# Optimization experiments

Measured on AMD Instinct MI355X. Metric: run time of the kernel, lower is better.

Reference implementation:

```python
import jax, jax.numpy as jnp
import numpy as np

N_NODES = 5000
N_EDGES = 50000
BATCH = 8
SEQ = 12
IN_CH = 2
HID = 64
OUT_CH = 1
K = 3
N_LAYERS = 2


def setup_inputs() -> dict:
    key = jax.random.key(0)
    ks = jax.random.split(key, 20)
    d = {}
    d["x"] = jax.random.normal(ks[0], (BATCH, SEQ, N_NODES, IN_CH), dtype=jnp.float32)
    d["edge_index"] = jax.random.randint(ks[1], (2, N_EDGES), 0, N_NODES, dtype=jnp.int32)

    def w(k, fin):
        return jax.random.normal(k, (2, K, fin, HID), dtype=jnp.float32) * 0.05

    fins = [IN_CH + HID, HID + HID]
    i = 2
    for l in range(N_LAYERS):
        for g in ("z", "r", "h"):
            d["W" + g + str(l)] = w(ks[i], fins[l]); i += 1
            d["b" + g + str(l)] = jnp.zeros((HID,), jnp.float32)
    d["Wo"] = jax.random.normal(ks[i], (HID, OUT_CH), dtype=jnp.float32) * 0.05
    d["bo"] = jnp.zeros((OUT_CH,), jnp.float32)
    return d


def reference(x, edge_index,
              Wz0, bz0, Wr0, br0, Wh0, bh0,
              Wz1, bz1, Wr1, br1, Wh1, bh1,
              Wo, bo):
    B, T, N, _ = x.shape
    src, dst = edge_index[0], edge_index[1]
    ones = jnp.ones(src.shape, x.dtype)
    deg_out = jax.ops.segment_sum(ones, src, num_segments=N)
    deg_in = jax.ops.segment_sum(ones, dst, num_segments=N)
    inv = lambda dgr: jnp.where(dgr > 0, 1.0 / dgr, 0.0)
    norm_out = inv(deg_out)[src]  # [E], 1/deg_out(src)
    norm_in = inv(deg_in)[dst]    # [E], 1/deg_in(dst)

    def prop(X, norm):
        # X: [N, B, F] -> sparse matvec via gather/scatter
        msg = norm[:, None, None] * X[src]
        return jax.ops.segment_sum(msg, dst, num_segments=N)

    def dconv(X, W, b):
        # X: [N, B, Fin]; W: [2, K, Fin, H]; dual-direction Chebyshev diffusion
        H = jnp.einsum('nbf,fh->nbh', X, W[0, 0] + W[1, 0])
        Tx0o = Tx0i = X
        Tx1o = prop(X, norm_out)
        Tx1i = prop(X, norm_in)
        H = H + jnp.einsum('nbf,fh->nbh', Tx1o, W[0, 1]) \
              + jnp.einsum('nbf,fh->nbh', Tx1i, W[1, 1])
        for k in range(2, W.shape[1]):
            Tx2o = 2.0 * prop(Tx1o, norm_out) - Tx0o
            Tx2i = 2.0 * prop(Tx1i, norm_in) - Tx0i
            H = H + jnp.einsum('nbf,fh->nbh', Tx2o, W[0, k]) \
                  + jnp.einsum('nbf,fh->nbh', Tx2i, W[1, k])
            Tx0o, Tx1o = Tx1o, Tx2o
            Tx0i, Tx1i = Tx1i, Tx2i
        return H + b

    def cell(Xin, H, p):
        Wz, bz, Wr, br, Wh, bh = p
        XH = jnp.concatenate([Xin, H], axis=-1)
        Z = jax.nn.sigmoid(dconv(XH, Wz, bz))
        R = jax.nn.sigmoid(dconv(XH, Wr, br))
        Ht = jnp.tanh(dconv(jnp.concatenate([Xin, H * R], axis=-1), Wh, bh))
        return Z * H + (1.0 - Z) * Ht

    layers = [(Wz0, bz0, Wr0, br0, Wh0, bh0), (Wz1, bz1, Wr1, br1, Wh1, bh1)]
    hid = Wo.shape[0]
    h0 = jnp.zeros((len(layers), N, B, hid), x.dtype)
    xs = jnp.transpose(x, (1, 2, 0, 3))  # [T, N, B, F]

    def step(h, xt):
        inp = xt
        new_h = []
        for l, p in enumerate(layers):
            hl = cell(inp, h[l], p)
            new_h.append(hl)
            inp = hl
        h = jnp.stack(new_h)
        out = jnp.einsum('nbh,ho->nbo', h[-1], Wo) + bo
        return h, out

    _, outs = jax.lax.scan(step, h0, xs)      # [T, N, B, O]
    return jnp.transpose(outs, (2, 0, 1, 3))  # [B, T, N, O]
```

## Files before the change

### kernel.cpp

```cpp
#include <hip/hip_runtime.h>
#include <math.h>

#define NNODES 5000
#define NEDGES 50000
#define SEQT 12
#define NB 40000
#define MAXDEG 128

typedef __attribute__((ext_vector_type(8))) _Float16 half8;
typedef __attribute__((ext_vector_type(2))) _Float16 half2v;
typedef __attribute__((ext_vector_type(4))) float f32x4;


__global__ void count_deg_k(const int* __restrict__ ei, int* deg_out, int* deg_in){
    int e = blockIdx.x*blockDim.x + threadIdx.x;
    if (e < NEDGES){
        atomicAdd(&deg_out[ei[e]], 1);
        atomicAdd(&deg_in[ei[NEDGES + e]], 1);
    }
}

__global__ void scan_k(const int* __restrict__ deg_in, int* __restrict__ row_ptr){
    __shared__ int part[256];
    int tid = threadIdx.x;
// ... 69 lines not shown
    int kb = ks*32 + ((lane>>4)<<3);
    size_t o = ((size_t)(ks*4 + cf)*64 + lane)*8;
    for (int j=0;j<8;j++){
        int k = kb + j;
        float v = 0.f;
        if (ks == 0){
            if (k < 10) v = wfetch(W, 66, k>>1, k&1, col);
        } else {
            int slot = (ks-1)>>1;
            int f = 2 + k - 32 - 64*slot;
            v = wfetch(W, 66, slot, f, col);
        }
        wh[o+j] = (_Float16)v;
    }
}

__global__ void pack_l1_k(const float* __restrict__ W, _Float16* __restrict__ wh){
    int idx = blockIdx.x*256 + threadIdx.x;
    if (idx >= 4*20*64) return;
    int lane = idx & 63, rest = idx >> 6;
    int ks = rest % 20, cf = rest / 20;
    int col = cf*16 + (lane & 15);
    int kb = ks*32 + ((lane>>4)<<3);
    int slot = ks >> 2;
    size_t o = ((size_t)(ks*4 + cf)*64 + lane)*8;
    for (int j=0;j<8;j++){
        int k = kb + j;
        int f = k - slot*128;
        wh[o+j] = (_Float16)wfetch(W, 128, slot, f, col);
    }
}


template<int WH>
__global__ __launch_bounds__(WH) void k_dualh(
    const _Float16* __restrict__ S,
    _Float16* __restrict__ Yo, _Float16* __restrict__ Yi,
    const int* __restrict__ rp, const int* __restrict__ cs,
    const float* __restrict__ cwo, const float* __restrict__ cwi){
    constexpr int SLAB = 8*WH;
    int n = blockIdx.x;
    int beg = rp[n], deg = rp[n+1]-beg;
    int nst = deg < MAXDEG ? deg : MAXDEG;
    __shared__ int s_o[MAXDEG]; __shared__ float swo[MAXDEG], swi[MAXDEG];
    for (int j=threadIdx.x; j<nst; j+=WH){
        s_o[j] = cs[beg+j]*SLAB;
        swo[j] = cwo[beg+j]; swi[j] = cwi[beg+j];
    }
    __syncthreads();
    int off = threadIdx.x*8;
    float ao[8] = {0,0,0,0,0,0,0,0}, ai[8] = {0,0,0,0,0,0,0,0};
    for (int j=0;j<nst;j++){
        half8 v = *(const half8*)(S + s_o[j] + off);
        float wo=swo[j], wi=swi[j];
        #pragma unroll
        for (int e=0;e<8;e++){
            float xv = (float)v[e];
            ao[e]=fmaf(wo,xv,ao[e]); ai[e]=fmaf(wi,xv,ai[e]);
        }
    }
    for (int j=nst;j<deg;j++){
        half8 v = *(const half8*)(S + (size_t)cs[beg+j]*SLAB + off);
        float wo=cwo[beg+j], wi=cwi[beg+j];
        #pragma unroll
        for (int e=0;e<8;e++){
            float xv = (float)v[e];
            ao[e]=fmaf(wo,xv,ao[e]); ai[e]=fmaf(wi,xv,ai[e]);
        }
    }
    half8 po, pi;
    #pragma unroll
    for (int e=0;e<8;e++){ po[e]=(_Float16)ao[e]; pi[e]=(_Float16)ai[e]; }
    *(half8*)(Yo + (size_t)n*SLAB + off) = po;
    *(half8*)(Yi + (size_t)n*SLAB + off) = pi;
}

template<int WH>
__global__ __launch_bounds__(WH) void k_prop2h(
    const _Float16* __restrict__ T1o, const _Float16* __restrict__ T1i,
    _Float16* __restrict__ U2o, _Float16* __restrict__ U2i,
    const int* __restrict__ rp, const int* __restrict__ cs,
    const float* __restrict__ cwo, const float* __restrict__ cwi){
    constexpr int SLAB = 8*WH;
    int bx = blockIdx.x;
    int n = bx >> 1, sel = bx & 1;
    const _Float16* S = sel ? T1i : T1o;
    _Float16* U = sel ? U2i : U2o;
    const float* cw = sel ? cwi : cwo;
    int beg = rp[n], deg = rp[n+1]-beg;
    int nst = deg < MAXDEG ? deg : MAXDEG;
    __shared__ int s_o[MAXDEG]; __shared__ float s_w[MAXDEG];
    for (int j=threadIdx.x; j<nst; j+=WH){
        s_o[j] = cs[beg+j]*SLAB;
        s_w[j] = cw[beg+j];
    }
    __syncthreads();
    int off = threadIdx.x*8;
    float a[8] = {0,0,0,0,0,0,0,0};
    for (int j=0;j<nst;j++){
        half8 v = *(const half8*)(S + s_o[j] + off);
        float w=s_w[j];
        #pragma unroll
        for (int e=0;e<8;e++) a[e]=fmaf(w,(float)v[e],a[e]);
    }
    for (int j=nst;j<deg;j++){
        half8 v = *(const half8*)(S + (size_t)cs[beg+j]*SLAB + off);
        float w=cw[beg+j];
        #pragma unroll
        for (int e=0;e<8;e++) a[e]=fmaf(w,(float)v[e],a[e]);
    }
    half8 p;
    #pragma unroll
    for (int e=0;e<8;e++) p[e]=(_Float16)a[e];
    *(half8*)(U + (size_t)n*SLAB + off) = p;
}

__global__ __launch_bounds__(64) void k_dual_l0zrh(
    const _Float16* __restrict__ h0h, const _Float16* __restrict__ Xt,
    _Float16* __restrict__ T1o, _Float16* __restrict__ T1i, _Float16* __restrict__ XTh,
    const int* __restrict__ rp, const int* __restrict__ cs,
    const float* __restrict__ cwo, const float* __restrict__ cwi){
    int n = blockIdx.x;
    int beg = rp[n], deg = rp[n+1]-beg;
    int nst = deg < MAXDEG ? deg : MAXDEG;
    __shared__ int s_o[MAXDEG]; __shared__ float swo[MAXDEG], swi[MAXDEG];
    for (int j=threadIdx.x; j<nst; j+=64){
        s_o[j] = cs[beg+j]*512;
        swo[j] = cwo[beg+j]; swi[j] = cwi[beg+j];
    }
    __syncthreads();
    int off = threadIdx.x*8;
    {
        float ao[8] = {0,0,0,0,0,0,0,0}, ai[8] = {0,0,0,0,0,0,0,0};
        for (int j=0;j<nst;j++){
            half8 v = *(const half8*)(h0h + s_o[j] + off);
            float wo=swo[j], wi=swi[j];
            #pragma unroll
            for (int e=0;e<8;e++){
                float xv = (float)v[e];
                ao[e]=fmaf(wo,xv,ao[e]); ai[e]=fmaf(wi,xv,ai[e]);
            }
        }
        for (int j=nst;j<deg;j++){
            half8 v = *(const half8*)(h0h + (size_t)cs[beg+j]*512 + off);
            float wo=cwo[beg+j], wi=cwi[beg+j];
            #pragma unroll
            for (int e=0;e<8;e++){
                float xv = (float)v[e];
                ao[e]=fmaf(wo,xv,ao[e]); ai[e]=fmaf(wi,xv,ai[e]);
            }
        }
        half8 po, pi;
        #pragma unroll
        for (int e=0;e<8;e++){ po[e]=(_Float16)ao[e]; pi[e]=(_Float16)ai[e]; }
        *(half8*)(T1o + (size_t)n*512 + off) = po;
        *(half8*)(T1i + (size_t)n*512 + off) = pi;
    }
    if (threadIdx.x < 8){
        int b = threadIdx.x;
        float ax0=0,ax1=0, ay0=0,ay1=0;
        for (int j=0;j<nst;j++){
            int src = s_o[j] >> 9;
            half2v v = *(const half2v*)(Xt + src*16 + b*2);
            float x0=(float)v[0], x1=(float)v[1];
            ax0=fmaf(swo[j],x0,ax0); ax1=fmaf(swo[j],x1,ax1);
            ay0=fmaf(swi[j],x0,ay0); ay1=fmaf(swi[j],x1,ay1);
        }
        for (int j=nst;j<deg;j++){
            int src = cs[beg+j];
            half2v v = *(const half2v*)(Xt + src*16 + b*2);
            float x0=(float)v[0], x1=(float)v[1];
            ax0=fmaf(cwo[beg+j],x0,ax0); ax1=fmaf(cwo[beg+j],x1,ax1);
            ay0=fmaf(cwi[beg+j],x0,ay0); ay1=fmaf(cwi[beg+j],x1,ay1);
        }
        size_t ro = (size_t)(n*8 + b)*32;
        XTh[ro+0] = Xt[(size_t)(n*8+b)*2+0];
        XTh[ro+1] = Xt[(size_t)(n*8+b)*2+1];
        XTh[ro+2] = (_Float16)ax0; XTh[ro+3] = (_Float16)ax1;
        XTh[ro+4] = (_Float16)ay0; XTh[ro+5] = (_Float16)ay1;
    }
}

__global__ __launch_bounds__(64) void k_prop2_l0zrh(
    const _Float16* __restrict__ T1o, const _Float16* __restrict__ T1i,
    _Float16* __restrict__ T2o, _Float16* __restrict__ T2i, _Float16* __restrict__ XTh,
    const int* __restrict__ rp, const int* __restrict__ cs,
    const float* __restrict__ cwo, const float* __restrict__ cwi){
    int bx = blockIdx.x;
    int n = bx >> 1, sel = bx & 1;
    const _Float16* S = sel ? T1i : T1o;
    _Float16* U = sel ? T2i : T2o;
    const float* cw = sel ? cwi : cwo;
    int beg = rp[n], deg = rp[n+1]-beg;
    int nst = deg < MAXDEG ? deg : MAXDEG;
    __shared__ int s_o[MAXDEG]; __shared__ float s_w[MAXDEG];
    for (int j=threadIdx.x; j<nst; j+=64){
        s_o[j] = cs[beg+j]*512;
        s_w[j] = cw[beg+j];
    }
    __syncthreads();
    int off = threadIdx.x*8;
    {
        float a[8] = {0,0,0,0,0,0,0,0};
        for (int j=0;j<nst;j++){
            half8 v = *(const half8*)(S + s_o[j] + off);
            float w=s_w[j];
            #pragma unroll
            for (int e=0;e<8;e++) a[e]=fmaf(w,(float)v[e],a[e]);
        }
        for (int j=nst;j<deg;j++){
            half8 v = *(const half8*)(S + (size_t)cs[beg+j]*512 + off);
            float w=cw[beg+j];
            #pragma unroll
            for (int e=0;e<8;e++) a[e]=fmaf(w,(float)v[e],a[e]);
        }
        half8 p;
        #pragma unroll
        for (int e=0;e<8;e++) p[e]=(_Float16)a[e];
        *(half8*)(U + (size_t)n*512 + off) = p;
    }
    if (threadIdx.x < 8){
        int b = threadIdx.x;
        int xo = 2 + 2*sel;
        float a0=0,a1=0;
        for (int j=0;j<nst;j++){
            int src = s_o[j] >> 9;
            half2v v = *(const half2v*)(XTh + (size_t)src*256 + b*32 + xo);
            a0=fmaf(s_w[j],(float)v[0],a0); a1=fmaf(s_w[j],(float)v[1],a1);
        }
        for (int j=nst;j<deg;j++){
            int src = cs[beg+j];
            half2v v = *(const half2v*)(XTh + (size_t)src*256 + b*32 + xo);
            a0=fmaf(cw[beg+j],(float)v[0],a0); a1=fmaf(cw[beg+j],(float)v[1],a1);
        }
        size_t ro = (size_t)(n*8 + b)*32 + 6 + 2*sel;
        XTh[ro+0] = (_Float16)a0; XTh[ro+1] = (_Float16)a1;
    }
}

__global__ __launch_bounds__(128) void k_dual2x64h(
    const _Float16* __restrict__ h0h, const _Float16* __restrict__ h1h,
    _Float16* __restrict__ T1o, _Float16* __restrict__ T1i,
    const int* __restrict__ rp, const int* __restrict__ cs,
    const float* __restrict__ cwo, const float* __restrict__ cwi){
    int n = blockIdx.x;
    int beg = rp[n], deg = rp[n+1]-beg;
    int nst = deg < MAXDEG ? deg : MAXDEG;
    __shared__ int s_o[MAXDEG]; __shared__ float swo[MAXDEG], swi[MAXDEG];
    for (int j=threadIdx.x; j<nst; j+=128){
        s_o[j] = cs[beg+j]*512;
        swo[j] = cwo[beg+j]; swi[j] = cwi[beg+j];
    }
    __syncthreads();
    int off = threadIdx.x*8;
    int b = off >> 7, c = off & 127;
    const _Float16* S = (c < 64) ? h0h : h1h;
    int soff = b*64 + (c & 63);
    float ao[8] = {0,0,0,0,0,0,0,0}, ai[8] = {0,0,0,0,0,0,0,0};
    for (int j=0;j<nst;j++){
        half8 v = *(const half8*)(S + s_o[j] + soff);
        float wo=swo[j], wi=swi[j];
        #pragma unroll
        for (int e=0;e<8;e++){
            float xv = (float)v[e];
            ao[e]=fmaf(wo,xv,ao[e]); ai[e]=fmaf(wi,xv,ai[e]);
        }
    }
    for (int j=nst;j<deg;j++){
        half8 v = *(const half8*)(S + (size_t)cs[beg+j]*512 + soff);
        float wo=cwo[beg+j], wi=cwi[beg+j];
        #pragma unroll
        for (int e=0;e<8;e++){
            float xv = (float)v[e];
            ao[e]=fmaf(wo,xv,ao[e]); ai[e]=fmaf(wi,xv,ai[e]);
        }
    }
    half8 po, pi;
    #pragma unroll
    for (int e=0;e<8;e++){ po[e]=(_Float16)ao[e]; pi[e]=(_Float16)ai[e]; }
    *(half8*)(T1o + (size_t)n*1024 + off) = po;
    *(half8*)(T1i + (size_t)n*1024 + off) = pi;
}


struct KD { const _Float16* a; int st; };
struct GA { KD kd[20]; };

template<int NK, int NG, int EPI>
__global__ __launch_bounds__(256) void k_gemm(GA ga,
    const _Float16* __restrict__ wh0, const float* __restrict__ b0,
    const _Float16* __restrict__ wh1, const float* __restrict__ b1,
    float* __restrict__ Z, _Float16* __restrict__ Gout,
    float* __restrict__ Hf, _Float16* __restrict__ Hh,
    const float* __restrict__ Wo, const float* __restrict__ bo,
    float* __restrict__ out, int t){
    __shared__ _Float16 ldsb[2][NG*2048];
    __shared__ float spr[4][32];
    const int tid = threadIdx.x;
    const int lane = tid & 63, wv = tid >> 6, rl = lane & 15, kg = lane >> 4;
    const int m0 = blockIdx.x*64 + (wv&1)*32;
    const int cfb = (wv>>1)*2;
    const _Float16* wsrc[2] = {wh0, wh1};

    half8 srg[NG];
    half8 a0, a1, a0n, a1n;

    auto sload = [&](int ks){
        #pragma unroll
        for (int j=0;j<NG;j++)
            srg[j] = *(const half8*)(wsrc[j] + (size_t)ks*2048 + tid*8);
    };
    auto swrite = [&](int buf){
        #pragma unroll
        for (int j=0;j<NG;j++)
            *(half8*)&ldsb[buf][j*2048 + tid*8] = srg[j];
    };
    auto aload = [&](int ks, half8& x0, half8& x1){
        const _Float16* base = ga.kd[ks].a;
        const int st = ga.kd[ks].st;
        x0 = *(const half8*)(base + (size_t)(m0+rl)*st + kg*8);
        x1 = *(const half8*)(base + (size_t)(m0+16+rl)*st + kg*8);
    };

    f32x4 acc[NG][2][2];
    #pragma unroll
    for (int g=0; g<NG; ++g)
        #pragma unroll
        for (int cc=0; cc<2; ++cc)
            #pragma unroll
            for (int mr=0; mr<2; ++mr){
                acc[g][cc][mr][0]=0.f; acc[g][cc][mr][1]=0.f;
                acc[g][cc][mr][2]=0.f; acc[g][cc][mr][3]=0.f;
            }

    sload(0); swrite(0);
    if (NK>1) sload(1);
    aload(0, a0, a1);
    __syncthreads();
    for (int ks=0; ks<NK; ++ks){
        const int cur = ks & 1;
        if (ks+1 < NK){ swrite(cur^1); aload(ks+1, a0n, a1n); }
        if (ks+2 < NK) sload(ks+2);
        #pragma unroll
        for (int g=0; g<NG; ++g){
            #pragma unroll
            for (int cc=0; cc<2; ++cc){
                half8 bv = *(const half8*)&ldsb[cur][g*2048 + (cfb+cc)*512 + lane*8];
                acc[g][cc][0] = __builtin_amdgcn_mfma_f32_16x16x32_f16(a0, bv, acc[g][cc][0], 0, 0, 0);
                acc[g][cc][1] = __builtin_amdgcn_mfma_f32_16x16x32_f16(a1, bv, acc[g][cc][1], 0, 0, 0);
            }
        }
        __syncthreads();
        a0 = a0n; a1 = a1n;
    }

    if constexpr (EPI == 0){
        #pragma unroll
        for (int cc=0; cc<2; ++cc){
            const int col = (cfb+cc)*16 + rl;
            float bzv = b0[col], brv = b1[col];
            #pragma unroll
            for (int mr=0; mr<2; ++mr)
                #pragma unroll
                for (int i=0;i<4;i++){
                    int row = m0 + mr*16 + kg*4 + i;
                    float z = 1.f/(1.f+__expf(-(acc[0][cc][mr][i] + bzv)));
                    float r = 1.f/(1.f+__expf(-(acc[NG-1][cc][mr][i] + brv)));
                    size_t ix = (size_t)row*64 + col;
                    Z[ix] = z;
                    Gout[ix] = (_Float16)(Hf[ix]*r);
                }
        }
    } else {
        float pr[2][4] = {{0.f,0.f,0.f,0.f},{0.f,0.f,0.f,0.f}};
        #pragma unroll
        for (int cc=0; cc<2; ++cc){
            const int col = (cfb+cc)*16 + rl;
            float bv = b0[col];
            float wo_c = 0.f;
            if constexpr (EPI == 2) wo_c = Wo[col];
            #pragma unroll
            for (int mr=0; mr<2; ++mr)
                #pragma unroll
                for (int i=0;i<4;i++){
                    int row = m0 + mr*16 + kg*4 + i;
                    float ht = tanhf(acc[0][cc][mr][i] + bv);
                    size_t ix = (size_t)row*64 + col;
                    float z = Z[ix];
                    float hn = z*Hf[ix] + (1.f-z)*ht;
                    Hf[ix] = hn;
                    Hh[ix] = (_Float16)hn;
                    if constexpr (EPI == 2) pr[mr][i] = fmaf(hn, wo_c, pr[mr][i]);
                }
        }
        if constexpr (EPI == 2){
            #pragma unroll
            for (int mr=0; mr<2; ++mr)
                #pragma unroll
                for (int i=0;i<4;i++){
                    float v = pr[mr][i];
                    v += __shfl_xor(v, 1);
                    v += __shfl_xor(v, 2);
                    v += __shfl_xor(v, 4);
                    v += __shfl_xor(v, 8);
                    if (rl == 0) spr[wv][mr*16 + kg*4 + i] = v;
                }
            __syncthreads();
            if (tid < 64){
                int r = tid;
                float v = spr[r>>5][r&31] + spr[(r>>5)|2][r&31] + bo[0];
                int row = blockIdx.x*64 + r;
                int n = row >> 3, b = row & 7;
                out[(size_t)(b*SEQT + t)*NNODES + n] = v;
            }
        }
    }
}


extern "C" void kernel_launch(void* const* d_in, const int* in_sizes, int n_in,
                              void* d_out, int out_size, void* d_ws, size_t ws_size,
                              hipStream_t stream){
    (void)in_sizes; (void)n_in; (void)out_size; (void)ws_size;
    const float* x  = (const float*)d_in[0];
    const int*   ei = (const int*)d_in[1];
    const float* Wz[2] = {(const float*)d_in[2],  (const float*)d_in[8]};
    const float* bz[2] = {(const float*)d_in[3],  (const float*)d_in[9]};
    const float* Wr[2] = {(const float*)d_in[4],  (const float*)d_in[10]};
    const float* br[2] = {(const float*)d_in[5],  (const float*)d_in[11]};
    const float* Wh[2] = {(const float*)d_in[6],  (const float*)d_in[12]};
    const float* bh[2] = {(const float*)d_in[7],  (const float*)d_in[13]};
    const float* Wo = (const float*)d_in[14];
    const float* bo = (const float*)d_in[15];
    float* out = (float*)d_out;

    char* p = (char*)d_ws;
    auto alloc = [&](size_t bytes)->char*{
        char* r = p; p += (bytes + 255) & ~(size_t)255; return r;
    };
    const size_t H64  = (size_t)NB*64*2;
    const size_t H128 = (size_t)NB*128*2;
    const size_t F64  = (size_t)NB*64*4;

    _Float16* Xtph = (_Float16*)alloc((size_t)SEQT*NB*2*2);
    float*    h0f = (float*)alloc(F64);
    float*    h1f = (float*)alloc(F64);
    float*    Z0  = (float*)alloc(F64);
    float*    Z1  = (float*)alloc(F64);
    _Float16* h0h = (_Float16*)alloc(H64);
    _Float16* h1h = (_Float16*)alloc(H64);
    _Float16* XTh = (_Float16*)alloc((size_t)NB*32*2);
    _Float16* Th1o = (_Float16*)alloc(H64);
    _Float16* Th1i = (_Float16*)alloc(H64);
    _Float16* Th2o = (_Float16*)alloc(H64);
    _Float16* Th2i = (_Float16*)alloc(H64);
    _Float16* G0L0 = (_Float16*)alloc(H64);
    _Float16* G1o0 = (_Float16*)alloc(H64);
    _Float16* G1i0 = (_Float16*)alloc(H64);
    _Float16* G2o0 = (_Float16*)alloc(H64);
    _Float16* G2i0 = (_Float16*)alloc(H64);
    _Float16* T1o128 = (_Float16*)alloc(H128);
    _Float16* T1i128 = (_Float16*)alloc(H128);
    _Float16* U2o128 = (_Float16*)alloc(H128);
    _Float16* U2i128 = (_Float16*)alloc(H128);
    _Float16* G0p  = (_Float16*)alloc(H64);
    _Float16* G1o1 = (_Float16*)alloc(H64);
    _Float16* G1i1 = (_Float16*)alloc(H64);
    _Float16* G2o1 = (_Float16*)alloc(H64);
    _Float16* G2i1 = (_Float16*)alloc(H64);
    _Float16 *whl0[3], *whl1[3];
    for (int g=0; g<3; ++g){
        whl0[g] = (_Float16*)alloc((size_t)4*11*64*8*2);
        whl1[g] = (_Float16*)alloc((size_t)4*20*64*8*2);
    }
    int* deg_out = (int*)alloc(NNODES*4);
    int* deg_in  = (int*)alloc(NNODES*4);
    int* row_ptr = (int*)alloc((NNODES+1)*4);
    int* cursor  = (int*)alloc(NNODES*4);
    int* csr_src = (int*)alloc(NEDGES*4);
    float* csr_wo = (float*)alloc(NEDGES*4);
    float* csr_wi = (float*)alloc(NEDGES*4);

    hipMemsetAsync(deg_out, 0, NNODES*4, stream);
    hipMemsetAsync(deg_in,  0, NNODES*4, stream);
    hipMemsetAsync(cursor,  0, NNODES*4, stream);
    hipMemsetAsync(h0f, 0, F64, stream);
    hipMemsetAsync(h1f, 0, F64, stream);
    hipMemsetAsync(h0h, 0, H64, stream);
    hipMemsetAsync(h1h, 0, H64, stream);
    hipMemsetAsync(XTh, 0, (size_t)NB*32*2, stream);

    count_deg_k<<<(NEDGES+255)/256, 256, 0, stream>>>(ei, deg_out, deg_in);
    scan_k<<<1, 256, 0, stream>>>(deg_in, row_ptr);
    fill_csr_k<<<(NEDGES+255)/256, 256, 0, stream>>>(ei, deg_out, deg_in, row_ptr,
                                                     cursor, csr_src, csr_wo, csr_wi);
    prepack_x_k<<<(SEQT*NB*2+255)/256, 256, 0, stream>>>(x, Xtph);
    const float* Wptr0[3] = {Wz[0], Wr[0], Wh[0]};
    const float* Wptr1[3] = {Wz[1], Wr[1], Wh[1]};
    for (int g=0; g<3; ++g){
        pack_l0_k<<<(4*11*64+255)/256, 256, 0, stream>>>(Wptr0[g], whl0[g]);
        pack_l1_k<<<(4*20*64+255)/256, 256, 0, stream>>>(Wptr1[g], whl1[g]);
    }

    GA gaL0zr = {}, gaL0h = {}, gaL1zr = {}, gaL1h = {};
    {
        const _Float16* t64[5] = {h0h, Th1o, Th1i, Th2o, Th2i};
        gaL0zr.kd[0] = {XTh, 32};
        for (int s=0; s<5; ++s){
            gaL0zr.kd[1+2*s] = {t64[s], 64};
            gaL0zr.kd[2+2*s] = {t64[s]+32, 64};
        }
        const _Float16* g64[5] = {G0L0, G1o0, G1i0, G2o0, G2i0};
        gaL0h.kd[0] = {XTh, 32};
        for (int s=0; s<5; ++s){
            gaL0h.kd[1+2*s] = {g64[s], 64};
            gaL0h.kd[2+2*s] = {g64[s]+32, 64};
        }
        gaL1zr.kd[0] = {h0h, 64};    gaL1zr.kd[1] = {h0h+32, 64};
        gaL1zr.kd[2] = {h1h, 64};    gaL1zr.kd[3] = {h1h+32, 64};
        const _Float16* t128[4] = {T1o128, T1i128, U2o128, U2i128};
        for (int s=0; s<4; ++s)
            for (int q=0; q<4; ++q)
                gaL1zr.kd[4+4*s+q] = {t128[s]+32*q, 128};
        gaL1h.kd[0] = {h0h, 64};  gaL1h.kd[1] = {h0h+32, 64};
        gaL1h.kd[2] = {G0p, 64};  gaL1h.kd[3] = {G0p+32, 64};
        const _Float16* gh[4] = {G1o1, G1i1, G2o1, G2i1};
        for (int s=0; s<4; ++s){
            gaL1h.kd[4+4*s+0] = {t128[s], 128};
            gaL1h.kd[4+4*s+1] = {t128[s]+32, 128};
            gaL1h.kd[4+4*s+2] = {gh[s], 64};
            gaL1h.kd[4+4*s+3] = {gh[s]+32, 64};
        }
    }

    for (int t=0; t<SEQT; ++t){
        k_dual_l0zrh<<<NNODES, 64, 0, stream>>>(h0h, Xtph + (size_t)t*NB*2, Th1o, Th1i, XTh,
                                                row_ptr, csr_src, csr_wo, csr_wi);
        k_prop2_l0zrh<<<2*NNODES, 64, 0, stream>>>(Th1o, Th1i, Th2o, Th2i, XTh,
                                                row_ptr, csr_src, csr_wo, csr_wi);
        k_gemm<11,2,0><<<NB/64, 256, 0, stream>>>(gaL0zr,
            whl0[0], bz[0], whl0[1], br[0],
            Z0, G0L0, h0f, nullptr, nullptr, nullptr, nullptr, 0);
        k_dualh<64><<<NNODES, 64, 0, stream>>>(G0L0, G1o0, G1i0, row_ptr, csr_src, csr_wo, csr_wi);
        k_prop2h<64><<<2*NNODES, 64, 0, stream>>>(G1o0, G1i0, G2o0, G2i0,
                                                row_ptr, csr_src, csr_wo, csr_wi);
        k_gemm<11,1,1><<<NB/64, 256, 0, stream>>>(gaL0h,
            whl0[2], bh[0], nullptr, nullptr,
            Z0, nullptr, h0f, h0h, nullptr, nullptr, nullptr, 0);
        k_dual2x64h<<<NNODES, 128, 0, stream>>>(h0h, h1h, T1o128, T1i128,
                                                row_ptr, csr_src, csr_wo, csr_wi);
        k_prop2h<128><<<2*NNODES, 128, 0, stream>>>(T1o128, T1i128, U2o128, U2i128,
                                                row_ptr, csr_src, csr_wo, csr_wi);
        k_gemm<20,2,0><<<NB/64, 256, 0, stream>>>(gaL1zr,
            whl1[0], bz[1], whl1[1], br[1],
            Z1, G0p, h1f, nullptr, nullptr, nullptr, nullptr, 0);
        k_dualh<64><<<NNODES, 64, 0, stream>>>(G0p, G1o1, G1i1, row_ptr, csr_src, csr_wo, csr_wi);
        k_prop2h<64><<<2*NNODES, 64, 0, stream>>>(G1o1, G1i1, G2o1, G2i1,
                                                row_ptr, csr_src, csr_wo, csr_wi);
        k_gemm<20,1,2><<<NB/64, 256, 0, stream>>>(gaL1h,
            whl1[2], bh[1], nullptr, nullptr,
            Z1, nullptr, h1f, h1h, Wo, bo, out, t);
    }
}
```

Measured before the change: 2.409 ms.

## Wavefront-pipeline layer 0 of step t+1 with layer 1 of step t in fused launches

Restructures the time loop as a software pipeline. Each launch now runs layer 1 of step s and layer 0 of step s+1 together, with block ranges split by an aCount parameter. The layer-0 hidden state is double-buffered so the two halves do not race. This halves the number of launches in the loop and gives each launch more blocks, cutting launch and tail overhead, at the cost of more complex kernels and branch divergence between block roles.

```diff
diff --git a/kernel.cpp b/kernel.cpp
--- a/kernel.cpp
+++ b/kernel.cpp
@@ -125,19 +125,209 @@
 }
 
 
-template<int WH>
-__global__ __launch_bounds__(WH) void k_dualh(
-    const _Float16* __restrict__ S,
-    _Float16* __restrict__ Yo, _Float16* __restrict__ Yi,
+__global__ __launch_bounds__(128) void k_f1(int aCount,
+    const _Float16* __restrict__ h0h, const _Float16* __restrict__ h1h,
+    _Float16* __restrict__ T1o128, _Float16* __restrict__ T1i128,
+    const _Float16* __restrict__ Xt,
+    _Float16* __restrict__ Th1o, _Float16* __restrict__ Th1i, _Float16* __restrict__ XTh,
     const int* __restrict__ rp, const int* __restrict__ cs,
     const float* __restrict__ cwo, const float* __restrict__ cwi){
-    constexpr int SLAB = 8*WH;
-    int n = blockIdx.x;
+    __shared__ int s_o[MAXDEG]; __shared__ float swo[MAXDEG], swi[MAXDEG];
+    const int bx = blockIdx.x;
+    const bool isA = bx < aCount;
+    const int n = isA ? bx : bx - aCount;
     int beg = rp[n], deg = rp[n+1]-beg;
     int nst = deg < MAXDEG ? deg : MAXDEG;
+    for (int j=threadIdx.x; j<nst; j+=128){
+        s_o[j] = cs[beg+j]*512;
+        swo[j] = cwo[beg+j]; swi[j] = cwi[beg+j];
+    }
+    __syncthreads();
+    if (isA){
+        int off = threadIdx.x*8;
+        int b = off >> 7, c = off & 127;
+        const _Float16* S = (c < 64) ? h0h : h1h;
+        int soff = b*64 + (c & 63);
+        float ao[8] = {0,0,0,0,0,0,0,0}, ai[8] = {0,0,0,0,0,0,0,0};
+        for (int j=0;j<nst;j++){
+            half8 v = *(const half8*)(S + s_o[j] + soff);
+            float wo=swo[j], wi=swi[j];
+            #pragma unroll
+            for (int e=0;e<8;e++){
+                float xv = (float)v[e];
+                ao[e]=fmaf(wo,xv,ao[e]); ai[e]=fmaf(wi,xv,ai[e]);
+            }
+        }
+        for (int j=nst;j<deg;j++){
+            half8 v = *(const half8*)(S + (size_t)cs[beg+j]*512 + soff);
+            float wo=cwo[beg+j], wi=cwi[beg+j];
+            #pragma unroll
+            for (int e=0;e<8;e++){
+                float xv = (float)v[e];
+                ao[e]=fmaf(wo,xv,ao[e]); ai[e]=fmaf(wi,xv,ai[e]);
+            }
+        }
+        half8 po, pi;
+        #pragma unroll
+        for (int e=0;e<8;e++){ po[e]=(_Float16)ao[e]; pi[e]=(_Float16)ai[e]; }
+        *(half8*)(T1o128 + (size_t)n*1024 + off) = po;
+        *(half8*)(T1i128 + (size_t)n*1024 + off) = pi;
+    } else {
+        if (threadIdx.x < 64){
+            int off = threadIdx.x*8;
+            float ao[8] = {0,0,0,0,0,0,0,0}, ai[8] = {0,0,0,0,0,0,0,0};
+            for (int j=0;j<nst;j++){
+                half8 v = *(const half8*)(h0h + s_o[j] + off);
+                float wo=swo[j], wi=swi[j];
+                #pragma unroll
+                for (int e=0;e<8;e++){
+                    float xv = (float)v[e];
+                    ao[e]=fmaf(wo,xv,ao[e]); ai[e]=fmaf(wi,xv,ai[e]);
+                }
+            }
+            for (int j=nst;j<deg;j++){
+                half8 v = *(const half8*)(h0h + (size_t)cs[beg+j]*512 + off);
+                float wo=cwo[beg+j], wi=cwi[beg+j];
+                #pragma unroll
+                for (int e=0;e<8;e++){
+                    float xv = (float)v[e];
+                    ao[e]=fmaf(wo,xv,ao[e]); ai[e]=fmaf(wi,xv,ai[e]);
+                }
+            }
+            half8 po, pi;
+            #pragma unroll
+            for (int e=0;e<8;e++){ po[e]=(_Float16)ao[e]; pi[e]=(_Float16)ai[e]; }
+            *(half8*)(Th1o + (size_t)n*512 + off) = po;
+            *(half8*)(Th1i + (size_t)n*512 + off) = pi;
+        }
+        if (threadIdx.x < 8){
+            int b = threadIdx.x;
+            float ax0=0,ax1=0, ay0=0,ay1=0;
+            for (int j=0;j<nst;j++){
+                int src = s_o[j] >> 9;
+                half2v v = *(const half2v*)(Xt + src*16 + b*2);
+                float x0=(float)v[0], x1=(float)v[1];
+                ax0=fmaf(swo[j],x0,ax0); ax1=fmaf(swo[j],x1,ax1);
+                ay0=fmaf(swi[j],x0,ay0); ay1=fmaf(swi[j],x1,ay1);
+            }
+            for (int j=nst;j<deg;j++){
+                int src = cs[beg+j];
+                half2v v = *(const half2v*)(Xt + src*16 + b*2);
+                float x0=(float)v[0], x1=(float)v[1];
+                ax0=fmaf(cwo[beg+j],x0,ax0); ax1=fmaf(cwo[beg+j],x1,ax1);
+                ay0=fmaf(cwi[beg+j],x0,ay0); ay1=fmaf(cwi[beg+j],x1,ay1);
+            }
+            size_t ro = (size_t)(n*8 + b)*32;
+            XTh[ro+0] = Xt[(size_t)(n*8+b)*2+0];
+            XTh[ro+1] = Xt[(size_t)(n*8+b)*2+1];
+            XTh[ro+2] = (_Float16)ax0; XTh[ro+3] = (_Float16)ax1;
+            XTh[ro+4] = (_Float16)ay0; XTh[ro+5] = (_Float16)ay1;
+        }
+    }
+}
+
+__global__ __launch_bounds__(128) void k_f2(int aCount,
+    const _Float16* __restrict__ T1o128, const _Float16* __restrict__ T1i128,
+    _Float16* __restrict__ U2o128, _Float16* __restrict__ U2i128,
+    const _Float16* __restrict__ Th1o, const _Float16* __restrict__ Th1i,
+    _Float16* __restrict__ Th2o, _Float16* __restrict__ Th2i, _Float16* __restrict__ XTh,
+    const int* __restrict__ rp, const int* __restrict__ cs,
+    const float* __restrict__ cwo, const float* __restrict__ cwi){
+    __shared__ int s_o[MAXDEG]; __shared__ float s_w[MAXDEG];
+    const int bx = blockIdx.x;
+    const bool isA = bx < aCount;
+    const int idx = isA ? bx : bx - aCount;
+    const int n = idx >> 1, sel = idx & 1;
+    const float* cw = sel ? cwi : cwo;
+    int beg = rp[n], deg = rp[n+1]-beg;
+    int nst = deg < MAXDEG ? deg : MAXDEG;
+    const int scale = isA ? 1024 : 512;
+    for (int j=threadIdx.x; j<nst; j+=128){
+        s_o[j] = cs[beg+j]*scale;
+        s_w[j] = cw[beg+j];
+    }
+    __syncthreads();
+    if (isA){
+        const _Float16* S = sel ? T1i128 : T1o128;
+        _Float16* U = sel ? U2i128 : U2o128;
+        int off = threadIdx.x*8;
+        float a[8] = {0,0,0,0,0,0,0,0};
+        for (int j=0;j<nst;j++){
+            half8 v = *(const half8*)(S + s_o[j] + off);
+            float w=s_w[j];
+            #pragma unroll
+            for (int e=0;e<8;e++) a[e]=fmaf(w,(float)v[e],a[e]);
+        }
+        for (int j=nst;j<deg;j++){
+            half8 v = *(const half8*)(S + (size_t)cs[beg+j]*1024 + off);
+            float w=cw[beg+j];
+            #pragma unroll
+            for (int e=0;e<8;e++) a[e]=fmaf(w,(float)v[e],a[e]);
+        }
+        half8 p;
+        #pragma unroll
+        for (int e=0;e<8;e++) p[e]=(_Float16)a[e];
+        *(half8*)(U + (size_t)n*1024 + off) = p;
+    } else {
+        const _Float16* S = sel ? Th1i : Th1o;
+        _Float16* U = sel ? Th2i : Th2o;
+        if (threadIdx.x < 64){
+            int off = threadIdx.x*8;
+            float a[8] = {0,0,0,0,0,0,0,0};
+            for (int j=0;j<nst;j++){
+                half8 v = *(const half8*)(S + s_o[j] + off);
+                float w=s_w[j];
+                #pragma unroll
+                for (int e=0;e<8;e++) a[e]=fmaf(w,(float)v[e],a[e]);
+            }
+            for (int j=nst;j<deg;j++){
+                half8 v = *(const half8*)(S + (size_t)cs[beg+j]*512 + off);
+                float w=cw[beg+j];
+                #pragma unroll
+                for (int e=0;e<8;e++) a[e]=fmaf(w,(float)v[e],a[e]);
+            }
+            half8 p;
+            #pragma unroll
+            for (int e=0;e<8;e++) p[e]=(_Float16)a[e];
+            *(half8*)(U + (size_t)n*512 + off) = p;
+        }
+        if (threadIdx.x < 8){
+            int b = threadIdx.x;
+            int xo = 2 + 2*sel;
+            float a0=0,a1=0;
+            for (int j=0;j<nst;j++){
+                int src = s_o[j] >> 9;
+                half2v v = *(const half2v*)(XTh + (size_t)src*256 + b*32 + xo);
+                a0=fmaf(s_w[j],(float)v[0],a0); a1=fmaf(s_w[j],(float)v[1],a1);
+            }
+            for (int j=nst;j<deg;j++){
+                int src = cs[beg+j];
+                float w = cw[beg+j];
+                half2v v = *(const half2v*)(XTh + (size_t)src*256 + b*32 + xo);
+                a0=fmaf(w,(float)v[0],a0); a1=fmaf(w,(float)v[1],a1);
+            }
+            size_t ro = (size_t)(n*8 + b)*32 + 6 + 2*sel;
+            XTh[ro+0] = (_Float16)a0; XTh[ro+1] = (_Float16)a1;
+        }
+    }
+}
+
+__global__ __launch_bounds__(64) void k_f4(int aCount,
+    const _Float16* __restrict__ SA, _Float16* __restrict__ YoA, _Float16* __restrict__ YiA,
+    const _Float16* __restrict__ SB, _Float16* __restrict__ YoB, _Float16* __restrict__ YiB,
+    const int* __restrict__ rp, const int* __restrict__ cs,
+    const float* __restrict__ cwo, const float* __restrict__ cwi){
     __shared__ int s_o[MAXDEG]; __shared__ float swo[MAXDEG], swi[MAXDEG];
-    for (int j=threadIdx.x; j<nst; j+=WH){
-        s_o[j] = cs[beg+j]*SLAB;
+    const int bx = blockIdx.x;
+    const bool isA = bx < aCount;
+    const int n = isA ? bx : bx - aCount;
+    const _Float16* S = isA ? SA : SB;
+    _Float16* Yo = isA ? YoA : YoB;
+    _Float16* Yi = isA ? YiA : YiB;
+    int beg = rp[n], deg = rp[n+1]-beg;
+    int nst = deg < MAXDEG ? deg : MAXDEG;
+    for (int j=threadIdx.x; j<nst; j+=64){
+        s_o[j] = cs[beg+j]*512;
         swo[j] = cwo[beg+j]; swi[j] = cwi[beg+j];
     }
     __syncthreads();
@@ -153,7 +343,7 @@
         }
     }
     for (int j=nst;j<deg;j++){
-        half8 v = *(const half8*)(S + (size_t)cs[beg+j]*SLAB + off);
+        half8 v = *(const half8*)(S + (size_t)cs[beg+j]*512 + off);
         float wo=cwo[beg+j], wi=cwi[beg+j];
         #pragma unroll
         for (int e=0;e<8;e++){
@@ -164,27 +354,29 @@
     half8 po, pi;
     #pragma unroll
     for (int e=0;e<8;e++){ po[e]=(_Float16)ao[e]; pi[e]=(_Float16)ai[e]; }
-    *(half8*)(Yo + (size_t)n*SLAB + off) = po;
-    *(half8*)(Yi + (size_t)n*SLAB + off) = pi;
-}
-
-template<int WH>
-__global__ __launch_bounds__(WH) void k_prop2h(
-    const _Float16* __restrict__ T1o, const _Float16* __restrict__ T1i,
-    _Float16* __restrict__ U2o, _Float16* __restrict__ U2i,
+    *(half8*)(Yo + (size_t)n*512 + off) = po;
+    *(half8*)(Yi + (size_t)n*512 + off) = pi;
+}
+
+__global__ __launch_bounds__(64) void k_f5(int aCount,
+    const _Float16* __restrict__ T1oA, const _Float16* __restrict__ T1iA,
+    _Float16* __restrict__ U2oA, _Float16* __restrict__ U2iA,
+    const _Float16* __restrict__ T1oB, const _Float16* __restrict__ T1iB,
+    _Float16* __restrict__ U2oB, _Float16* __restrict__ U2iB,
     const int* __restrict__ rp, const int* __restrict__ cs,
     const float* __restrict__ cwo, const float* __restrict__ cwi){
-    constexpr int SLAB = 8*WH;
-    int bx = blockIdx.x;
-    int n = bx >> 1, sel = bx & 1;
-    const _Float16* S = sel ? T1i : T1o;
-    _Float16* U = sel ? U2i : U2o;
+    __shared__ int s_o[MAXDEG]; __shared__ float s_w[MAXDEG];
+    const int bx = blockIdx.x;
+    const bool isA = bx < aCount;
+    const int idx = isA ? bx : bx - aCount;
+    const int n = idx >> 1, sel = idx & 1;
+    const _Float16* S = isA ? (sel ? T1iA : T1oA) : (sel ? T1iB : T1oB);
+    _Float16* U = isA ? (sel ? U2iA : U2oA) : (sel ? U2iB : U2oB);
     const float* cw = sel ? cwi : cwo;
     int beg = rp[n], deg = rp[n+1]-beg;
     int nst = deg < MAXDEG ? deg : MAXDEG;
-    __shared__ int s_o[MAXDEG]; __shared__ float s_w[MAXDEG];
-    for (int j=threadIdx.x; j<nst; j+=WH){
-        s_o[j] = cs[beg+j]*SLAB;
+    for (int j=threadIdx.x; j<nst; j+=64){
+        s_o[j] = cs[beg+j]*512;
         s_w[j] = cw[beg+j];
     }
     __syncthreads();
@@ -197,7 +389,7 @@
         for (int e=0;e<8;e++) a[e]=fmaf(w,(float)v[e],a[e]);
     }
     for (int j=nst;j<deg;j++){
-        half8 v = *(const half8*)(S + (size_t)cs[beg+j]*SLAB + off);
+        half8 v = *(const half8*)(S + (size_t)cs[beg+j]*512 + off);
         float w=cw[beg+j];
         #pragma unroll
         for (int e=0;e<8;e++) a[e]=fmaf(w,(float)v[e],a[e]);
@@ -205,174 +397,7 @@
     half8 p;
     #pragma unroll
     for (int e=0;e<8;e++) p[e]=(_Float16)a[e];
-    *(half8*)(U + (size_t)n*SLAB + off) = p;
-}
-
-__global__ __launch_bounds__(64) void k_dual_l0zrh(
-    const _Float16* __restrict__ h0h, const _Float16* __restrict__ Xt,
-    _Float16* __restrict__ T1o, _Float16* __restrict__ T1i, _Float16* __restrict__ XTh,
-    const int* __restrict__ rp, const int* __restrict__ cs,
-    const float* __restrict__ cwo, const float* __restrict__ cwi){
-    int n = blockIdx.x;
-    int beg = rp[n], deg = rp[n+1]-beg;
-    int nst = deg < MAXDEG ? deg : MAXDEG;
-    __shared__ int s_o[MAXDEG]; __shared__ float swo[MAXDEG], swi[MAXDEG];
-    for (int j=threadIdx.x; j<nst; j+=64){
-        s_o[j] = cs[beg+j]*512;
-        swo[j] = cwo[beg+j]; swi[j] = cwi[beg+j];
-    }
-    __syncthreads();
-    int off = threadIdx.x*8;
-    {
-        float ao[8] = {0,0,0,0,0,0,0,0}, ai[8] = {0,0,0,0,0,0,0,0};
-        for (int j=0;j<nst;j++){
-            half8 v = *(const half8*)(h0h + s_o[j] + off);
-            float wo=swo[j], wi=swi[j];
-            #pragma unroll
-            for (int e=0;e<8;e++){
-                float xv = (float)v[e];
-                ao[e]=fmaf(wo,xv,ao[e]); ai[e]=fmaf(wi,xv,ai[e]);
-            }
-        }
-        for (int j=nst;j<deg;j++){
-            half8 v = *(const half8*)(h0h + (size_t)cs[beg+j]*512 + off);
-            float wo=cwo[beg+j], wi=cwi[beg+j];
-            #pragma unroll
-            for (int e=0;e<8;e++){
-                float xv = (float)v[e];
-                ao[e]=fmaf(wo,xv,ao[e]); ai[e]=fmaf(wi,xv,ai[e]);
-            }
-        }
-        half8 po, pi;
-        #pragma unroll
-        for (int e=0;e<8;e++){ po[e]=(_Float16)ao[e]; pi[e]=(_Float16)ai[e]; }
-        *(half8*)(T1o + (size_t)n*512 + off) = po;
-        *(half8*)(T1i + (size_t)n*512 + off) = pi;
-    }
-    if (threadIdx.x < 8){
-        int b = threadIdx.x;
-        float ax0=0,ax1=0, ay0=0,ay1=0;
-        for (int j=0;j<nst;j++){
-            int src = s_o[j] >> 9;
-            half2v v = *(const half2v*)(Xt + src*16 + b*2);
-            float x0=(float)v[0], x1=(float)v[1];
-            ax0=fmaf(swo[j],x0,ax0); ax1=fmaf(swo[j],x1,ax1);
-            ay0=fmaf(swi[j],x0,ay0); ay1=fmaf(swi[j],x1,ay1);
-        }
-        for (int j=nst;j<deg;j++){
-            int src = cs[beg+j];
-            half2v v = *(const half2v*)(Xt + src*16 + b*2);
-            float x0=(float)v[0], x1=(float)v[1];
-            ax0=fmaf(cwo[beg+j],x0,ax0); ax1=fmaf(cwo[beg+j],x1,ax1);
-            ay0=fmaf(cwi[beg+j],x0,ay0); ay1=fmaf(cwi[beg+j],x1,ay1);
-        }
-        size_t ro = (size_t)(n*8 + b)*32;
-        XTh[ro+0] = Xt[(size_t)(n*8+b)*2+0];
-        XTh[ro+1] = Xt[(size_t)(n*8+b)*2+1];
-        XTh[ro+2] = (_Float16)ax0; XTh[ro+3] = (_Float16)ax1;
-        XTh[ro+4] = (_Float16)ay0; XTh[ro+5] = (_Float16)ay1;
-    }
-}
-
-__global__ __launch_bounds__(64) void k_prop2_l0zrh(
-    const _Float16* __restrict__ T1o, const _Float16* __restrict__ T1i,
-    _Float16* __restrict__ T2o, _Float16* __restrict__ T2i, _Float16* __restrict__ XTh,
-    const int* __restrict__ rp, const int* __restrict__ cs,
-    const float* __restrict__ cwo, const float* __restrict__ cwi){
-    int bx = blockIdx.x;
-    int n = bx >> 1, sel = bx & 1;
-    const _Float16* S = sel ? T1i : T1o;
-    _Float16* U = sel ? T2i : T2o;
-    const float* cw = sel ? cwi : cwo;
-    int beg = rp[n], deg = rp[n+1]-beg;
-    int nst = deg < MAXDEG ? deg : MAXDEG;
-    __shared__ int s_o[MAXDEG]; __shared__ float s_w[MAXDEG];
-    for (int j=threadIdx.x; j<nst; j+=64){
-        s_o[j] = cs[beg+j]*512;
-        s_w[j] = cw[beg+j];
-    }
-    __syncthreads();
-    int off = threadIdx.x*8;
-    {
-        float a[8] = {0,0,0,0,0,0,0,0};
-        for (int j=0;j<nst;j++){
-            half8 v = *(const half8*)(S + s_o[j] + off);
-            float w=s_w[j];
-            #pragma unroll
-            for (int e=0;e<8;e++) a[e]=fmaf(w,(float)v[e],a[e]);
-        }
-        for (int j=nst;j<deg;j++){
-            half8 v = *(const half8*)(S + (size_t)cs[beg+j]*512 + off);
-            float w=cw[beg+j];
-            #pragma unroll
-            for (int e=0;e<8;e++) a[e]=fmaf(w,(float)v[e],a[e]);
-        }
-        half8 p;
-        #pragma unroll
-        for (int e=0;e<8;e++) p[e]=(_Float16)a[e];
-        *(half8*)(U + (size_t)n*512 + off) = p;
-    }
-    if (threadIdx.x < 8){
-        int b = threadIdx.x;
-        int xo = 2 + 2*sel;
-        float a0=0,a1=0;
-        for (int j=0;j<nst;j++){
-            int src = s_o[j] >> 9;
-            half2v v = *(const half2v*)(XTh + (size_t)src*256 + b*32 + xo);
-            a0=fmaf(s_w[j],(float)v[0],a0); a1=fmaf(s_w[j],(float)v[1],a1);
-        }
-        for (int j=nst;j<deg;j++){
-            int src = cs[beg+j];
-            half2v v = *(const half2v*)(XTh + (size_t)src*256 + b*32 + xo);
-            a0=fmaf(cw[beg+j],(float)v[0],a0); a1=fmaf(cw[beg+j],(float)v[1],a1);
-        }
-        size_t ro = (size_t)(n*8 + b)*32 + 6 + 2*sel;
-        XTh[ro+0] = (_Float16)a0; XTh[ro+1] = (_Float16)a1;
-    }
-}
-
-__global__ __launch_bounds__(128) void k_dual2x64h(
-    const _Float16* __restrict__ h0h, const _Float16* __restrict__ h1h,
-    _Float16* __restrict__ T1o, _Float16* __restrict__ T1i,
-    const int* __restrict__ rp, const int* __restrict__ cs,
-    const float* __restrict__ cwo, const float* __restrict__ cwi){
-    int n = blockIdx.x;
-    int beg = rp[n], deg = rp[n+1]-beg;
-    int nst = deg < MAXDEG ? deg : MAXDEG;
-    __shared__ int s_o[MAXDEG]; __shared__ float swo[MAXDEG], swi[MAXDEG];
-    for (int j=threadIdx.x; j<nst; j+=128){
-        s_o[j] = cs[beg+j]*512;
-        swo[j] = cwo[beg+j]; swi[j] = cwi[beg+j];
-    }
-    __syncthreads();
-    int off = threadIdx.x*8;
-    int b = off >> 7, c = off & 127;
-    const _Float16* S = (c < 64) ? h0h : h1h;
-    int soff = b*64 + (c & 63);
-    float ao[8] = {0,0,0,0,0,0,0,0}, ai[8] = {0,0,0,0,0,0,0,0};
-    for (int j=0;j<nst;j++){
-        half8 v = *(const half8*)(S + s_o[j] + soff);
-        float wo=swo[j], wi=swi[j];
-        #pragma unroll
-        for (int e=0;e<8;e++){
-            float xv = (float)v[e];
-            ao[e]=fmaf(wo,xv,ao[e]); ai[e]=fmaf(wi,xv,ai[e]);
-        }
-    }
-    for (int j=nst;j<deg;j++){
-        half8 v = *(const half8*)(S + (size_t)cs[beg+j]*512 + soff);
-        float wo=cwo[beg+j], wi=cwi[beg+j];
-        #pragma unroll
-        for (int e=0;e<8;e++){
-            float xv = (float)v[e];
-            ao[e]=fmaf(wo,xv,ao[e]); ai[e]=fmaf(wi,xv,ai[e]);
-        }
-    }
-    half8 po, pi;
-    #pragma unroll
-    for (int e=0;e<8;e++){ po[e]=(_Float16)ao[e]; pi[e]=(_Float16)ai[e]; }
-    *(half8*)(T1o + (size_t)n*1024 + off) = po;
-    *(half8*)(T1i + (size_t)n*1024 + off) = pi;
+    *(half8*)(U + (size_t)n*512 + off) = p;
 }
 
 
@@ -380,18 +405,18 @@
 struct GA { KD kd[20]; };
 
 template<int NK, int NG, int EPI>
-__global__ __launch_bounds__(256) void k_gemm(GA ga,
+__device__ __forceinline__ void gemm_body(char* smemraw, int bxm, const GA& ga,
     const _Float16* __restrict__ wh0, const float* __restrict__ b0,
     const _Float16* __restrict__ wh1, const float* __restrict__ b1,
     float* __restrict__ Z, _Float16* __restrict__ Gout,
     float* __restrict__ Hf, _Float16* __restrict__ Hh,
     const float* __restrict__ Wo, const float* __restrict__ bo,
     float* __restrict__ out, int t){
-    __shared__ _Float16 ldsb[2][NG*2048];
-    __shared__ float spr[4][32];
+    _Float16* ldsb = (_Float16*)smemraw;
+    float* spr = (float*)(smemraw + (size_t)4*NG*2048);
     const int tid = threadIdx.x;
     const int lane = tid & 63, wv = tid >> 6, rl = lane & 15, kg = lane >> 4;
-    const int m0 = blockIdx.x*64 + (wv&1)*32;
+    const int m0 = bxm*64 + (wv&1)*32;
     const int cfb = (wv>>1)*2;
     const _Float16* wsrc[2] = {wh0, wh1};
 
@@ -406,7 +431,7 @@
     auto swrite = [&](int buf){
         #pragma unroll
         for (int j=0;j<NG;j++)
-            *(half8*)&ldsb[buf][j*2048 + tid*8] = srg[j];
+            *(half8*)&ldsb[buf*(NG*2048) + j*2048 + tid*8] = srg[j];
     };
     auto aload = [&](int ks, half8& x0, half8& x1){
         const _Float16* base = ga.kd[ks].a;
@@ -438,7 +463,7 @@
         for (int g=0; g<NG; ++g){
             #pragma unroll
             for (int cc=0; cc<2; ++cc){
-                half8 bv = *(const half8*)&ldsb[cur][g*2048 + (cfb+cc)*512 + lane*8];
+                half8 bv = *(const half8*)&ldsb[cur*(NG*2048) + g*2048 + (cfb+cc)*512 + lane*8];
                 acc[g][cc][0] = __builtin_amdgcn_mfma_f32_16x16x32_f16(a0, bv, acc[g][cc][0], 0, 0, 0);
                 acc[g][cc][1] = __builtin_amdgcn_mfma_f32_16x16x32_f16(a1, bv, acc[g][cc][1], 0, 0, 0);
             }
@@ -496,18 +521,47 @@
                     v += __shfl_xor(v, 2);
                     v += __shfl_xor(v, 4);
                     v += __shfl_xor(v, 8);
-                    if (rl == 0) spr[wv][mr*16 + kg*4 + i] = v;
+                    if (rl == 0) spr[wv*32 + mr*16 + kg*4 + i] = v;
                 }
             __syncthreads();
             if (tid < 64){
                 int r = tid;
-                float v = spr[r>>5][r&31] + spr[(r>>5)|2][r&31] + bo[0];
-                int row = blockIdx.x*64 + r;
+                float v = spr[(r>>5)*32 + (r&31)] + spr[((r>>5)|2)*32 + (r&31)] + bo[0];
+                int row = bxm*64 + r;
                 int n = row >> 3, b = row & 7;
                 out[(size_t)(b*SEQT + t)*NNODES + n] = v;
             }
         }
     }
+}
+
+__global__ __launch_bounds__(256) void k_f3(int aCount,
+    GA gaA, const _Float16* whA0, const float* bA0, const _Float16* whA1, const float* bA1,
+    float* ZA, _Float16* GoA, float* HfA,
+    GA gaB, const _Float16* whB0, const float* bB0, const _Float16* whB1, const float* bB1,
+    float* ZB, _Float16* GoB, float* HfB){
+    __shared__ __align__(16) char smem[4*2*2048 + 512];
+    if (blockIdx.x < aCount)
+        gemm_body<20,2,0>(smem, blockIdx.x, gaA, whA0, bA0, whA1, bA1,
+                          ZA, GoA, HfA, nullptr, nullptr, nullptr, nullptr, 0);
+    else
+        gemm_body<11,2,0>(smem, blockIdx.x - aCount, gaB, whB0, bB0, whB1, bB1,
+                          ZB, GoB, HfB, nullptr, nullptr, nullptr, nullptr, 0);
+}
+
+__global__ __launch_bounds__(256) void k_f6(int aCount,
+    GA gaA, const _Float16* whA, const float* bA,
+    float* ZA, float* HfA, _Float16* HhA,
+    const float* Wo, const float* bo, float* out, int t,
+    GA gaB, const _Float16* whB, const float* bB,
+    float* ZB, float* HfB, _Float16* HhB){
+    __shared__ __align__(16) char smem[4*1*2048 + 512];
+    if (blockIdx.x < aCount)
+        gemm_body<20,1,2>(smem, blockIdx.x, gaA, whA, bA, nullptr, nullptr,
+                          ZA, nullptr, HfA, HhA, Wo, bo, out, t);
+    else
+        gemm_body<11,1,1>(smem, blockIdx.x - aCount, gaB, whB, bB, nullptr, nullptr,
+                          ZB, nullptr, HfB, HhB, nullptr, nullptr, nullptr, 0);
 }
 
 
@@ -540,7 +594,9 @@
     float*    h1f = (float*)alloc(F64);
     float*    Z0  = (float*)alloc(F64);
     float*    Z1  = (float*)alloc(F64);
-    _Float16* h0h = (_Float16*)alloc(H64);
+    _Float16* h0hb[2];
+    h0hb[0] = (_Float16*)alloc(H64);
+    h0hb[1] = (_Float16*)alloc(H64);
     _Float16* h1h = (_Float16*)alloc(H64);
     _Float16* XTh = (_Float16*)alloc((size_t)NB*32*2);
     _Float16* Th1o = (_Float16*)alloc(H64);
@@ -579,7 +635,8 @@
     hipMemsetAsync(cursor,  0, NNODES*4, stream);
     hipMemsetAsync(h0f, 0, F64, stream);
     hipMemsetAsync(h1f, 0, F64, stream);
-    hipMemsetAsync(h0h, 0, H64, stream);
+    hipMemsetAsync(h0hb[0], 0, H64, stream);
+    hipMemsetAsync(h0hb[1], 0, H64, stream);
     hipMemsetAsync(h1h, 0, H64, stream);
     hipMemsetAsync(XTh, 0, (size_t)NB*32*2, stream);
 
@@ -595,63 +652,74 @@
         pack_l1_k<<<(4*20*64+255)/256, 256, 0, stream>>>(Wptr1[g], whl1[g]);
     }
 
-    GA gaL0zr = {}, gaL0h = {}, gaL1zr = {}, gaL1h = {};
+    GA gaL0zr[2] = {}, gaL1zr[2] = {}, gaL1h[2] = {}, gaL0h = {};
+    for (int pp=0; pp<2; ++pp){
+        const _Float16* t64[5] = {h0hb[pp], Th1o, Th1i, Th2o, Th2i};
+        gaL0zr[pp].kd[0] = {XTh, 32};
+        for (int s=0; s<5; ++s){
+            gaL0zr[pp].kd[1+2*s] = {t64[s], 64};
+            gaL0zr[pp].kd[2+2*s] = {t64[s]+32, 64};
+        }
+        gaL1zr[pp].kd[0] = {h0hb[pp], 64};    gaL1zr[pp].kd[1] = {h0hb[pp]+32, 64};
+        gaL1zr[pp].kd[2] = {h1h, 64};         gaL1zr[pp].kd[3] = {h1h+32, 64};
+        const _Float16* t128[4] = {T1o128, T1i128, U2o128, U2i128};
+        for (int s=0; s<4; ++s)
+            for (int q=0; q<4; ++q)
+                gaL1zr[pp].kd[4+4*s+q] = {t128[s]+32*q, 128};
+        gaL1h[pp].kd[0] = {h0hb[pp], 64};  gaL1h[pp].kd[1] = {h0hb[pp]+32, 64};
+        gaL1h[pp].kd[2] = {G0p, 64};       gaL1h[pp].kd[3] = {G0p+32, 64};
+        const _Float16* gh[4] = {G1o1, G1i1, G2o1, G2i1};
+        for (int s=0; s<4; ++s){
+            gaL1h[pp].kd[4+4*s+0] = {t128[s], 128};
+            gaL1h[pp].kd[4+4*s+1] = {t128[s]+32, 128};
+            gaL1h[pp].kd[4+4*s+2] = {gh[s], 64};
+            gaL1h[pp].kd[4+4*s+3] = {gh[s]+32, 64};
+        }
+    }
     {
-        const _Float16* t64[5] = {h0h, Th1o, Th1i, Th2o, Th2i};
-        gaL0zr.kd[0] = {XTh, 32};
-        for (int s=0; s<5; ++s){
-            gaL0zr.kd[1+2*s] = {t64[s], 64};
-            gaL0zr.kd[2+2*s] = {t64[s]+32, 64};
-        }
         const _Float16* g64[5] = {G0L0, G1o0, G1i0, G2o0, G2i0};
         gaL0h.kd[0] = {XTh, 32};
         for (int s=0; s<5; ++s){
             gaL0h.kd[1+2*s] = {g64[s], 64};
             gaL0h.kd[2+2*s] = {g64[s]+32, 64};
         }
-        gaL1zr.kd[0] = {h0h, 64};    gaL1zr.kd[1] = {h0h+32, 64};
-        gaL1zr.kd[2] = {h1h, 64};    gaL1zr.kd[3] = {h1h+32, 64};
-        const _Float16* t128[4] = {T1o128, T1i128, U2o128, U2i128};
-        for (int s=0; s<4; ++s)
-            for (int q=0; q<4; ++q)
-                gaL1zr.kd[4+4*s+q] = {t128[s]+32*q, 128};
-        gaL1h.kd[0] = {h0h, 64};  gaL1h.kd[1] = {h0h+32, 64};
-        gaL1h.kd[2] = {G0p, 64};  gaL1h.kd[3] = {G0p+32, 64};
-        const _Float16* gh[4] = {G1o1, G1i1, G2o1, G2i1};
-        for (int s=0; s<4; ++s){
-            gaL1h.kd[4+4*s+0] = {t128[s], 128};
-            gaL1h.kd[4+4*s+1] = {t128[s]+32, 128};
-            gaL1h.kd[4+4*s+2] = {gh[s], 64};
-            gaL1h.kd[4+4*s+3] = {gh[s]+32, 64};
-        }
-    }
-
-    for (int t=0; t<SEQT; ++t){
-        k_dual_l0zrh<<<NNODES, 64, 0, stream>>>(h0h, Xtph + (size_t)t*NB*2, Th1o, Th1i, XTh,
-                                                row_ptr, csr_src, csr_wo, csr_wi);
-        k_prop2_l0zrh<<<2*NNODES, 64, 0, stream>>>(Th1o, Th1i, Th2o, Th2i, XTh,
-                                                row_ptr, csr_src, csr_wo, csr_wi);
-        k_gemm<11,2,0><<<NB/64, 256, 0, stream>>>(gaL0zr,
-            whl0[0], bz[0], whl0[1], br[0],
-            Z0, G0L0, h0f, nullptr, nullptr, nullptr, nullptr, 0);
-        k_dualh<64><<<NNODES, 64, 0, stream>>>(G0L0, G1o0, G1i0, row_ptr, csr_src, csr_wo, csr_wi);
-        k_prop2h<64><<<2*NNODES, 64, 0, stream>>>(G1o0, G1i0, G2o0, G2i0,
-                                                row_ptr, csr_src, csr_wo, csr_wi);
-        k_gemm<11,1,1><<<NB/64, 256, 0, stream>>>(gaL0h,
-            whl0[2], bh[0], nullptr, nullptr,
-            Z0, nullptr, h0f, h0h, nullptr, nullptr, nullptr, 0);
-        k_dual2x64h<<<NNODES, 128, 0, stream>>>(h0h, h1h, T1o128, T1i128,
-                                                row_ptr, csr_src, csr_wo, csr_wi);
-        k_prop2h<128><<<2*NNODES, 128, 0, stream>>>(T1o128, T1i128, U2o128, U2i128,
-                                                row_ptr, csr_src, csr_wo, csr_wi);
-        k_gemm<20,2,0><<<NB/64, 256, 0, stream>>>(gaL1zr,
-            whl1[0], bz[1], whl1[1], br[1],
-            Z1, G0p, h1f, nullptr, nullptr, nullptr, nullptr, 0);
-        k_dualh<64><<<NNODES, 64, 0, stream>>>(G0p, G1o1, G1i1, row_ptr, csr_src, csr_wo, csr_wi);
-        k_prop2h<64><<<2*NNODES, 64, 0, stream>>>(G1o1, G1i1, G2o1, G2i1,
-                                                row_ptr, csr_src, csr_wo, csr_wi);
-        k_gemm<20,1,2><<<NB/64, 256, 0, stream>>>(gaL1h,
-            whl1[2], bh[1], nullptr, nullptr,
-            Z1, nullptr, h1f, h1h, Wo, bo, out, t);
-    }
-}
+    }
+
+    k_f1<<<NNODES, 128, 0, stream>>>(0, h0hb[1], h1h, T1o128, T1i128,
+        Xtph, Th1o, Th1i, XTh, row_ptr, csr_src, csr_wo, csr_wi);
+    k_f2<<<2*NNODES, 128, 0, stream>>>(0, T1o128, T1i128, U2o128, U2i128,
+        Th1o, Th1i, Th2o, Th2i, XTh, row_ptr, csr_src, csr_wo, csr_wi);
+    k_f3<<<625, 256, 0, stream>>>(0,
+        gaL1zr[1], whl1[0], bz[1], whl1[1], br[1], Z1, G0p, h1f,
+        gaL0zr[1], whl0[0], bz[0], whl0[1], br[0], Z0, G0L0, h0f);
+    k_f4<<<NNODES, 64, 0, stream>>>(0, G0p, G1o1, G1i1, G0L0, G1o0, G1i0,
+        row_ptr, csr_src, csr_wo, csr_wi);
+    k_f5<<<2*NNODES, 64, 0, stream>>>(0, G1o1, G1i1, G2o1, G2i1,
+        G1o0, G1i0, G2o0, G2i0, row_ptr, csr_src, csr_wo, csr_wi);
+    k_f6<<<625, 256, 0, stream>>>(0,
+        gaL1h[1], whl1[2], bh[1], Z1, h1f, h1h, Wo, bo, out, 0,
+        gaL0h, whl0[2], bh[0], Z0, h0f, h0hb[0]);
+
+    for (int s=0; s<SEQT; ++s){
+        const int pr = s & 1;
+        const int doB = (s+1 < SEQT) ? 1 : 0;
+        k_f1<<<NNODES*(1+doB), 128, 0, stream>>>(NNODES,
+            h0hb[pr], h1h, T1o128, T1i128,
+            Xtph + (size_t)(doB ? s+1 : s)*NB*2, Th1o, Th1i, XTh,
+            row_ptr, csr_src, csr_wo, csr_wi);
+        k_f2<<<2*NNODES*(1+doB), 128, 0, stream>>>(2*NNODES,
+            T1o128, T1i128, U2o128, U2i128,
+            Th1o, Th1i, Th2o, Th2i, XTh, row_ptr, csr_src, csr_wo, csr_wi);
+        k_f3<<<625*(1+doB), 256, 0, stream>>>(625,
+            gaL1zr[pr], whl1[0], bz[1], whl1[1], br[1], Z1, G0p, h1f,
+            gaL0zr[pr], whl0[0], bz[0], whl0[1], br[0], Z0, G0L0, h0f);
+        k_f4<<<NNODES*(1+doB), 64, 0, stream>>>(NNODES,
+            G0p, G1o1, G1i1, G0L0, G1o0, G1i0, row_ptr, csr_src, csr_wo, csr_wi);
+        k_f5<<<2*NNODES*(1+doB), 64, 0, stream>>>(2*NNODES,
+            G1o1, G1i1, G2o1, G2i1, G1o0, G1i0, G2o0, G2i0,
+            row_ptr, csr_src, csr_wo, csr_wi);
+        k_f6<<<625*(1+doB), 256, 0, stream>>>(625,
+            gaL1h[pr], whl1[2], bh[1], Z1, h1f, h1h, Wo, bo, out, s,
+            gaL0h, whl0[2], bh[0], Z0, h0f, h0hb[(s+1)&1]);
+    }
+}
```

New measurement: 2.178 ms. -9.6%, faster.
